# Kernel optimization log

Measured on AMD Instinct MI355X. Metric: run time of the kernel, lower is better.

The kernel has to match this reference:

```python
import jax, jax.numpy as jnp
import numpy as np

NUM_HEADS = 8
NUM_GROUPS = 32
EPS = 1e-5


def setup_inputs() -> dict:
    key = jax.random.key(0)
    k1, k2, k3 = jax.random.split(key, 3)
    B, C, H, W = 2, 512, 64, 64
    x = jax.random.normal(k1, (B, C, H, W), dtype=jnp.float32)
    gn_weight = jnp.ones((C,), dtype=jnp.float32)
    gn_bias = jnp.zeros((C,), dtype=jnp.float32)
    # small init so softmax logits are well-conditioned
    w_qkv = jax.random.normal(k2, (3 * C, C), dtype=jnp.float32) * 0.02
    w_proj = jax.random.normal(k3, (C, C), dtype=jnp.float32) * 0.02
    b_proj = jnp.zeros((C,), dtype=jnp.float32)
    return {"x": x, "gn_weight": gn_weight, "gn_bias": gn_bias,
            "w_qkv": w_qkv, "w_proj": w_proj, "b_proj": b_proj}


def group_norm(x, weight, bias):
    B, C, H, W = x.shape
    xg = x.reshape(B, NUM_GROUPS, C // NUM_GROUPS, H, W)
    mean = xg.mean(axis=(2, 3, 4), keepdims=True)
    var = xg.var(axis=(2, 3, 4), keepdims=True)
    xg = (xg - mean) * jax.lax.rsqrt(var + EPS)
    x = xg.reshape(B, C, H, W)
    return x * weight[None, :, None, None] + bias[None, :, None, None]


def reference(x, gn_weight, gn_bias, w_qkv, w_proj, b_proj):
    B, C, H, W = x.shape
    nh = NUM_HEADS
    hd = C // nh
    N = H * W

    h = group_norm(x, gn_weight, gn_bias)
    # 1x1 conv == per-pixel matmul: [B,3C,H,W]
    qkv = jnp.einsum('bchw,oc->bohw', h, w_qkv)
    # (B,3,nh,hd,N) -> (3,B,nh,N,hd)
    qkv = qkv.reshape(B, 3, nh, hd, N).transpose(1, 0, 2, 4, 3)
    q, k, v = qkv[0], qkv[1], qkv[2]

    scale = hd ** -0.5
    attn = jax.nn.softmax(jnp.einsum('bhnd,bhmd->bhnm', q, k) * scale, axis=-1)
    out = jnp.einsum('bhnm,bhmd->bhnd', attn, v)  # [B,nh,N,hd]
    out = out.transpose(0, 1, 3, 2).reshape(B, C, H, W)
    out = jnp.einsum('bchw,oc->bohw', out, w_proj) + b_proj[None, :, None, None]
    return x + out
```

## Files before the change

kernel.cpp:

```cpp
#include <hip/hip_runtime.h>
#include <math.h>

#define BB 2
#define CC 512
#define NN 4096
#define NH 8
#define HD 64
#define NG 32
#define CPG 16

typedef __attribute__((ext_vector_type(8))) short short8;
typedef __attribute__((ext_vector_type(4))) float f32x4;
typedef __attribute__((ext_vector_type(16))) float f32x16;

typedef __attribute__((address_space(1))) void glb_t;
typedef __attribute__((address_space(3))) void lds_t;

__device__ __forceinline__ void async16(const void* g, void* l) {
  __builtin_amdgcn_global_load_lds((const glb_t*)g, (lds_t*)l, 16, 0, 0);
}

__device__ __forceinline__ unsigned short f2bf(float f) {
  unsigned int u = __float_as_uint(f);
  u += 0x7fffu + ((u >> 16) & 1u);
  return (unsigned short)(u >> 16);
}

__device__ __forceinline__ unsigned int cvt_pk_bf16(float a, float b) {
  unsigned int r;
  asm("v_cvt_pk_bf16_f32 %0, %1, %2" : "=v"(r) : "v"(a), "v"(b));
  return r;
}

__global__ __launch_bounds__(256) void k_pre(const float* __restrict__ x,
                                             const float* __restrict__ wqkv,
                                             const float* __restrict__ wproj,
                                             float* __restrict__ stats,
                                             unsigned short* __restrict__ wb) {
  int bid = blockIdx.x;
  if (bid >= 64) {
    int i = ((bid - 64) * 256 + threadIdx.x) * 4;
    const float* src = (i < 786432) ? (wqkv + i) : (wproj + (i - 786432));
    float4 v = *(const float4*)src;
    ushort4 o;
    o.x = f2bf(v.x); o.y = f2bf(v.y); o.z = f2bf(v.z); o.w = f2bf(v.w);
    *(ushort4*)(wb + i) = o;
    return;
  }
  int b = bid >> 5, g = bid & 31;
  const float4* p = (const float4*)(x + (size_t)(b * CC + g * CPG) * NN);
  double s = 0.0, sq = 0.0;
  for (int i = threadIdx.x; i < (CPG * NN) / 4; i += 256) {
    float4 v = p[i];
    s  += (double)v.x + (double)v.y + (double)v.z + (double)v.w;
    sq += (double)v.x * v.x + (double)v.y * v.y + (double)v.z * v.z + (double)v.w * v.w;
  }
  __shared__ double red[512];
  red[threadIdx.x] = s; red[256 + threadIdx.x] = sq;
  __syncthreads();
  for (int off = 128; off > 0; off >>= 1) {
    if (threadIdx.x < off) {
      red[threadIdx.x] += red[threadIdx.x + off];
      red[256 + threadIdx.x] += red[256 + threadIdx.x + off];
    }
    __syncthreads();
  }
  if (threadIdx.x == 0) {
    double mean = red[0] / (double)(CPG * NN);
    double var  = red[256] / (double)(CPG * NN) - mean * mean;
    stats[(b * NG + g) * 2]     = (float)mean;
    stats[(b * NG + g) * 2 + 1] = (float)(1.0 / sqrt(var + 1e-5));
  }
}

__global__ __launch_bounds__(256) void k_gnapply(const float* __restrict__ x,
                                                 const float* __restrict__ gw,
                                                 const float* __restrict__ gb,
                                                 const float* __restrict__ stats,
                                                 unsigned short* __restrict__ hT) {
  int bid = blockIdx.x;
  int b = bid >> 9;
  int c0 = ((bid >> 6) & 7) * 64;
  int n0 = (bid & 63) * 64;
  __shared__ float tile[64 * 68];
  int t = threadIdx.x;
#pragma unroll
  for (int i = 0; i < 4; ++i) {
    int idx = i * 256 + t;
    int c = idx >> 4, n4 = (idx & 15) * 4;
    int cg = c0 + c, g = cg >> 4;
    float mu = stats[(b * NG + g) * 2], rs = stats[(b * NG + g) * 2 + 1];
    float w = gw[cg], bb = gb[cg];
    float4 v = *(const float4*)(x + (size_t)(b * CC + cg) * NN + n0 + n4);
    float* dst = tile + c * 68 + n4;
    dst[0] = (v.x - mu) * rs * w + bb;
    dst[1] = (v.y - mu) * rs * w + bb;
    dst[2] = (v.z - mu) * rs * w + bb;
    dst[3] = (v.w - mu) * rs * w + bb;
  }
  __syncthreads();
#pragma unroll
  for (int i = 0; i < 2; ++i) {
    int idx = i * 256 + t;
    int n = idx >> 3, c8 = (idx & 7) * 8;
    short8 o;
#pragma unroll
    for (int j = 0; j < 8; ++j) o[j] = (short)f2bf(tile[(c8 + j) * 68 + n]);
    *(short8*)(hT + (size_t)(b * NN + n0 + n) * CC + c0 + c8) = o;
  }
}

__device__ __forceinline__ void gemm_mainloop(const unsigned short* __restrict__ A,
                                              const unsigned short* __restrict__ Bm,
                                              char* smem, int m0, int n0,
                                              f32x4 acc[4][4]) {
  const int t = threadIdx.x, wave = t >> 6, lane = t & 63;
  const int l15 = lane & 15, lhi = lane >> 4;
  const int wr = wave >> 1, wc = wave & 1;
  const f32x4 fz = {0.f, 0.f, 0.f, 0.f};
#pragma unroll
  for (int mi = 0; mi < 4; ++mi)
#pragma unroll
    for (int ni = 0; ni < 4; ++ni) acc[mi][ni] = fz;

  for (int kt = 0; kt < 8; ++kt) {
    __syncthreads();
#pragma unroll
    for (int issue = 0; issue < 4; ++issue) {
      int slot = issue * 256 + t;
      int row = slot >> 3, g = slot & 7;
      async16(A + (size_t)(m0 + row) * 512 + kt * 64 + g * 8,
              smem + issue * 4096 + wave * 1024);
      async16(Bm + (size_t)(n0 + row) * 512 + kt * 64 + g * 8,
              smem + 16384 + issue * 4096 + wave * 1024);
    }
    __syncthreads();
#pragma unroll
    for (int kk = 0; kk < 2; ++kk) {
      short8 a[4], bf[4];
#pragma unroll
      for (int mi = 0; mi < 4; ++mi)
        a[mi] = *(const short8*)(smem + (wr * 64 + mi * 16 + l15) * 128 + kk * 64 + lhi * 16);
#pragma unroll
      for (int ni = 0; ni < 4; ++ni)
        bf[ni] = *(const short8*)(smem + 16384 + (wc * 64 + ni * 16 + l15) * 128 + kk * 64 + lhi * 16);
#pragma unroll
      for (int mi = 0; mi < 4; ++mi)
#pragma unroll
        for (int ni = 0; ni < 4; ++ni)
          acc[mi][ni] = __builtin_amdgcn_mfma_f32_16x16x32_bf16(a[mi], bf[ni], acc[mi][ni], 0, 0, 0);
    }
  }
}

__global__ __launch_bounds__(256) void k_qkvgemm(const unsigned short* __restrict__ hT,
                                                 const unsigned short* __restrict__ Wq,
                                                 unsigned short* __restrict__ Qp,
                                                 unsigned short* __restrict__ Kp,
                                                 unsigned short* __restrict__ Vp) {
  __shared__ char smem[32768];
  f32x4 acc[4][4];
  int m0 = blockIdx.x * 128, n0 = blockIdx.y * 128;
  gemm_mainloop(hT, Wq, smem, m0, n0, acc);
  const int t = threadIdx.x, wave = t >> 6, lane = t & 63;
  const int l15 = lane & 15, lhi = lane >> 4;
  const int wr = wave >> 1, wc = wave & 1;
  const int type = n0 >> 9;
  const int h0 = (n0 >> 6) & 7;
  __syncthreads();
  unsigned short* lim = (unsigned short*)smem;
  const float qs = 0.18033688011112042f;
#pragma unroll
  for (int mi = 0; mi < 4; ++mi)
#pragma unroll
    for (int ni = 0; ni < 4; ++ni)
#pragma unroll
      for (int r = 0; r < 4; ++r) {
        int pr = wr * 64 + mi * 16 + lhi * 4 + r;
        int oc = wc * 64 + ni * 16 + l15;
        int hh = oc >> 6, c = oc & 63;
        int tt2 = pr >> 6, pn = pr & 63;
        int idx;
        if (type < 2)
          idx = ((hh * 2 + tt2) * 8 + ((pn >> 5) << 2) + (c >> 4)) * 512
              + ((c >> 3) & 1) * 256 + (pn & 31) * 8 + (c & 7);
        else
          idx = ((hh * 2 + tt2) * 8 + ((pn >> 5) << 2) + (((pn >> 4) & 1) << 1) + (c >> 5)) * 512
              + ((pn >> 3) & 1) * 256 + (c & 31) * 8 + (pn & 7);
        float v = acc[mi][ni][r];
        if (type == 0) v *= qs;
        lim[idx] = f2bf(v);
      }
  __syncthreads();
  unsigned short* gbp = type == 0 ? Qp : (type == 1 ? Kp : Vp);
  int b = m0 >> 12, tile0 = (m0 & 4095) >> 6;
#pragma unroll
  for (int i = 0; i < 8; ++i) {
    int cidx = i * 256 + t;
    int pg = cidx >> 6;
    int bh = b * 8 + h0 + (pg >> 4);
    size_t dst = (size_t)bh * 262144 + (size_t)(tile0 + ((pg >> 3) & 1)) * 4096
               + (size_t)(pg & 7) * 512 + (size_t)(cidx & 63) * 8;
    *(short8*)(gbp + dst) = *(const short8*)(lim + cidx * 8);
  }
}

__global__ __launch_bounds__(256) void k_attn(const unsigned short* __restrict__ Qp,
                                              const unsigned short* __restrict__ Kp,
                                              const unsigned short* __restrict__ Vp,
                                              unsigned short* __restrict__ att) {
  __shared__ char smem[32768];
  const int t = threadIdx.x, wave = t >> 6, lane = t & 63;
  const int l31 = lane & 31, lh = lane >> 5;
  const int wq = wave >> 1, wk = wave & 1;
  int bid0 = blockIdx.x;
  int bid = (bid0 & 7) * 128 + (bid0 >> 3);
  int bh = bid >> 6, qt = bid & 63;
  int b = bh >> 3, h = bh & 7;

  const char* kCur = (const char*)Kp + (size_t)bh * 524288;
  const char* vCur = (const char*)Vp + (size_t)bh * 524288;
  const char* qSrc = (const char*)Qp + (size_t)bh * 524288 + (size_t)qt * 8192;

#pragma unroll
  for (int i = 0; i < 2; ++i) {
    int p = i * 4 + wave;
    async16(qSrc + p * 1024 + lane * 16, smem + 16384 + p * 1024);
    async16(kCur + p * 1024 + lane * 16, smem + p * 1024);
    async16(vCur + p * 1024 + lane * 16, smem + 8192 + p * 1024);
  }
  kCur += 8192; vCur += 8192;

  const int rbK = wk * 4096 + lane * 16;
  const int rbV = 8192 + wk * 4096 + lane * 16;
  const int rbQ = 16384 + wq * 4096 + lane * 16;

  __syncthreads();
  short8 qa[4];
#pragma unroll
  for (int kk = 0; kk < 4; ++kk)
    qa[kk] = *(const short8*)(smem + rbQ + kk * 1024);
  __syncthreads();

  f32x16 o0 = (f32x16)0.f, o1 = (f32x16)0.f;
  float lsum = 0.f;

#define ATTN_BODY(CURB, NXTB)                                                          \
  {                                                                                    \
    _Pragma("unroll")                                                                  \
    for (int i = 0; i < 2; ++i) {                                                      \
      int p = i * 4 + wave;                                                            \
      async16(kCur + p * 1024 + lane * 16, smem + (NXTB) + p * 1024);                  \
      async16(vCur + p * 1024 + lane * 16, smem + (NXTB) + 8192 + p * 1024);           \
    }                                                                                  \
    kCur += 8192; vCur += 8192;                                                        \
    f32x16 sT = (f32x16)0.f;                                                           \
    __builtin_amdgcn_s_setprio(1);                                                     \
    _Pragma("unroll")                                                                  \
    for (int kk = 0; kk < 4; ++kk) {                                                   \
      short8 ka = *(const short8*)(smem + (CURB) + rbK + kk * 1024);                   \
      sT = __builtin_amdgcn_mfma_f32_32x32x16_bf16(ka, qa[kk], sT, 0, 0, 0);           \
    }                                                                                  \
    __builtin_amdgcn_s_setprio(0);                                                     \
    float ls0 = 0.f, ls1 = 0.f;                                                        \
    _Pragma("unroll")                                                                  \
    for (int r = 0; r < 16; r += 2) {                                                  \
      sT[r]     = __builtin_amdgcn_exp2f(sT[r]);                                       \
      sT[r + 1] = __builtin_amdgcn_exp2f(sT[r + 1]);                                   \
      ls0 += sT[r]; ls1 += sT[r + 1];                                                  \
    }                                                                                  \
    lsum += ls0 + ls1;                                                                 \
    __builtin_amdgcn_s_setprio(1);                                                     \
    _Pragma("unroll")                                                                  \
    for (int kc = 0; kc < 2; ++kc) {                                                   \
      int rb = kc * 8;                                                                 \
      unsigned int x0 = cvt_pk_bf16(sT[rb],     sT[rb + 1]);                           \
      unsigned int x1 = cvt_pk_bf16(sT[rb + 2], sT[rb + 3]);                           \
      unsigned int x2 = cvt_pk_bf16(sT[rb + 4], sT[rb + 5]);                           \
      unsigned int x3 = cvt_pk_bf16(sT[rb + 6], sT[rb + 7]);                           \
      asm("v_permlane32_swap_b32 %0, %1" : "+v"(x0), "+v"(x2));                        \
      asm("v_permlane32_swap_b32 %0, %1" : "+v"(x1), "+v"(x3));                        \
      union { unsigned int d[4]; short8 s; } pb;                                       \
      pb.d[0] = x0; pb.d[1] = x1; pb.d[2] = x2; pb.d[3] = x3;                          \
      short8 va0 = *(const short8*)(smem + (CURB) + rbV + kc * 2048);                  \
      o0 = __builtin_amdgcn_mfma_f32_32x32x16_bf16(va0, pb.s, o0, 0, 0, 0);            \
      short8 va1 = *(const short8*)(smem + (CURB) + rbV + kc * 2048 + 1024);           \
      o1 = __builtin_amdgcn_mfma_f32_32x32x16_bf16(va1, pb.s, o1, 0, 0, 0);            \
    }                                                                                  \
    __builtin_amdgcn_s_setprio(0);                                                     \
    __syncthreads();                                                                   \
  }

  for (int it2 = 0; it2 < 32; ++it2) {
    ATTN_BODY(0, 16384)
    ATTN_BODY(16384, 0)
  }
#undef ATTN_BODY

  lsum += __shfl_xor(lsum, 32, 64);
  if (wk) {
    char* os = smem + wq * 8192;
#pragma unroll
    for (int dt = 0; dt < 2; ++dt)
#pragma unroll
      for (int rp = 0; rp < 4; ++rp) {
        f32x4 v;
        v[0] = (dt ? o1 : o0)[4 * rp];     v[1] = (dt ? o1 : o0)[4 * rp + 1];
        v[2] = (dt ? o1 : o0)[4 * rp + 2]; v[3] = (dt ? o1 : o0)[4 * rp + 3];
        *(f32x4*)(os + (dt * 4 + rp) * 1024 + lane * 16) = v;
      }
    *(float*)(smem + 16384 + wq * 256 + lane * 4) = lsum;
  }
  __syncthreads();
  if (!wk) {
    float lt = lsum + *(const float*)(smem + 16384 + wq * 256 + lane * 4);
    float rl = 1.f / lt;
    const char* os = smem + wq * 8192;
#pragma unroll
    for (int dt = 0; dt < 2; ++dt)
#pragma unroll
      for (int rp = 0; rp < 4; ++rp) {
        f32x4 v = *(const f32x4*)(os + (dt * 4 + rp) * 1024 + lane * 16);
        if (dt) {
          o1[4 * rp] += v[0]; o1[4 * rp + 1] += v[1];
          o1[4 * rp + 2] += v[2]; o1[4 * rp + 3] += v[3];
        } else {
          o0[4 * rp] += v[0]; o0[4 * rp + 1] += v[1];
          o0[4 * rp + 2] += v[2]; o0[4 * rp + 3] += v[3];
        }
      }
    unsigned short* abase = att + (size_t)(b * NN + qt * 64 + wq * 32 + l31) * CC + h * 64 + 4 * lh;
#pragma unroll
    for (int dt = 0; dt < 2; ++dt)
#pragma unroll
      for (int rp = 0; rp < 8; ++rp) {
        float e0 = (dt ? o1 : o0)[2 * rp], e1 = (dt ? o1 : o0)[2 * rp + 1];
        unsigned int w = cvt_pk_bf16(e0 * rl, e1 * rl);
        *(unsigned int*)(abase + 32 * dt + 8 * (rp >> 1) + 2 * (rp & 1)) = w;
      }
  }
}

__global__ __launch_bounds__(256) void k_projgemm(const unsigned short* __restrict__ att,
                                                  const unsigned short* __restrict__ Wp,
                                                  const float* __restrict__ x,
                                                  const float* __restrict__ bproj,
                                                  float* __restrict__ out) {
  __shared__ char smem[33280];
  f32x4 acc[4][4];
  int m0 = blockIdx.x * 128, n0 = blockIdx.y * 128;
  gemm_mainloop(att, Wp, smem, m0, n0, acc);
  const int t = threadIdx.x, wave = t >> 6, lane = t & 63;
  const int l15 = lane & 15, lhi = lane >> 4;
  const int wr = wave >> 1, wc = wave & 1;
  __syncthreads();
  float* stg = (float*)(smem + wave * 8320);
  int b = m0 >> 12;
  int nbase = (m0 & 4095) + wr * 64;
#pragma unroll
  for (int half = 0; half < 2; ++half) {
#pragma unroll
    for (int nl = 0; nl < 2; ++nl) {
      int ni = half * 2 + nl;
#pragma unroll
      for (int mi = 0; mi < 4; ++mi)
#pragma unroll
        for (int r = 0; r < 4; ++r) {
          int cl = nl * 16 + l15;
          int row = mi * 16 + lhi * 4 + r;
          stg[cl * 65 + row] = acc[mi][ni][r];
        }
    }
#pragma unroll 4
    for (int i = 0; i < 32; ++i) {
      int oc = n0 + wc * 64 + half * 32 + i;
      float v = stg[i * 65 + lane];
      size_t idx = (size_t)(b * CC + oc) * NN + nbase + lane;
      out[idx] = x[idx] + v + bproj[oc];
    }
    __syncthreads();
  }
}

extern "C" void kernel_launch(void* const* d_in, const int* in_sizes, int n_in,
                              void* d_out, int out_size, void* d_ws, size_t ws_size,
                              hipStream_t stream) {
  const float* x     = (const float*)d_in[0];
  const float* gw    = (const float*)d_in[1];
  const float* gb    = (const float*)d_in[2];
  const float* wqkv  = (const float*)d_in[3];
  const float* wproj = (const float*)d_in[4];
  const float* bproj = (const float*)d_in[5];
  float* out = (float*)d_out;
  char* ws = (char*)d_ws;

  unsigned short* Qp     = (unsigned short*)(ws + 0);
  unsigned short* Kp     = (unsigned short*)(ws + 8388608);
  unsigned short* Vp     = (unsigned short*)(ws + 16777216);
  unsigned short* hTb    = (unsigned short*)(ws + 25165824);
  unsigned short* attb   = (unsigned short*)(ws + 25165824);
  unsigned short* wqkvb  = (unsigned short*)(ws + 33554432);
  unsigned short* wprojb = (unsigned short*)(ws + 35127296);
  float*          stats  = (float*)(ws + 35651584);

  k_pre<<<1088, 256, 0, stream>>>(x, wqkv, wproj, stats, wqkvb);
  k_gnapply<<<1024, 256, 0, stream>>>(x, gw, gb, stats, hTb);
  k_qkvgemm<<<dim3(64, 12), 256, 0, stream>>>(hTb, wqkvb, Qp, Kp, Vp);
  k_attn<<<1024, 256, 0, stream>>>(Qp, Kp, Vp, attb);
  k_projgemm<<<dim3(64, 4), 256, 0, stream>>>(attb, wprojb, x, bproj, out);
}
```

Measured before the change: 235.8 us.

## Restructure attention: per-wave private K/V buffers, 64 queries per wave, no block barriers

Each wave now streams its own half of K/V into a private double-buffered LDS region and processes two 32-row query tiles (A and B) against each loaded K/V chunk. That halves the K/V traffic per query and drops the per-iteration __syncthreads, relying on explicit vmcnt/lgkmcnt waits instead. The grid is halved to 512 blocks, each covering 128 queries, and LDS grows to about 68KB with launch bounds targeting 2 blocks per CU. The cost is higher register pressure from four accumulators, fewer resident waves, and the risk that the hand-placed waitcnt ordering is fragile.

```diff
diff --git a/kernel.cpp b/kernel.cpp
--- a/kernel.cpp
+++ b/kernel.cpp
@@ -205,139 +205,189 @@
   }
 }
 
-__global__ __launch_bounds__(256) void k_attn(const unsigned short* __restrict__ Qp,
-                                              const unsigned short* __restrict__ Kp,
-                                              const unsigned short* __restrict__ Vp,
-                                              unsigned short* __restrict__ att) {
-  __shared__ char smem[32768];
+__global__ __launch_bounds__(256, 2) void k_attn(const unsigned short* __restrict__ Qp,
+                                                 const unsigned short* __restrict__ Kp,
+                                                 const unsigned short* __restrict__ Vp,
+                                                 unsigned short* __restrict__ att) {
+  __shared__ char smem[69632];
   const int t = threadIdx.x, wave = t >> 6, lane = t & 63;
   const int l31 = lane & 31, lh = lane >> 5;
-  const int wq = wave >> 1, wk = wave & 1;
+  const int qw = wave >> 1, wk = wave & 1;
   int bid0 = blockIdx.x;
-  int bid = (bid0 & 7) * 128 + (bid0 >> 3);
-  int bh = bid >> 6, qt = bid & 63;
+  int xcd = bid0 & 7, rr = bid0 >> 3;
+  int bh = xcd * 2 + (rr >> 5), qp = rr & 31;
+  int qt = qp * 2 + qw;
   int b = bh >> 3, h = bh & 7;
 
-  const char* kCur = (const char*)Kp + (size_t)bh * 524288;
-  const char* vCur = (const char*)Vp + (size_t)bh * 524288;
-  const char* qSrc = (const char*)Qp + (size_t)bh * 524288 + (size_t)qt * 8192;
-
-#pragma unroll
-  for (int i = 0; i < 2; ++i) {
-    int p = i * 4 + wave;
-    async16(qSrc + p * 1024 + lane * 16, smem + 16384 + p * 1024);
-    async16(kCur + p * 1024 + lane * 16, smem + p * 1024);
-    async16(vCur + p * 1024 + lane * 16, smem + 8192 + p * 1024);
-  }
-  kCur += 8192; vCur += 8192;
-
-  const int rbK = wk * 4096 + lane * 16;
-  const int rbV = 8192 + wk * 4096 + lane * 16;
-  const int rbQ = 16384 + wq * 4096 + lane * 16;
-
-  __syncthreads();
-  short8 qa[4];
-#pragma unroll
-  for (int kk = 0; kk < 4; ++kk)
-    qa[kk] = *(const short8*)(smem + rbQ + kk * 1024);
-  __syncthreads();
-
-  f32x16 o0 = (f32x16)0.f, o1 = (f32x16)0.f;
-  float lsum = 0.f;
-
-#define ATTN_BODY(CURB, NXTB)                                                          \
+  char* myLds = smem + wave * 16384;
+  const char* kPtr = (const char*)Kp + (size_t)bh * 524288 + wk * 4096 + lane * 16;
+  const char* vPtr = (const char*)Vp + (size_t)bh * 524288 + wk * 4096 + lane * 16;
+  const char* qPtr = (const char*)Qp + (size_t)bh * 524288 + (size_t)qt * 8192 + lane * 16;
+
+#pragma unroll
+  for (int j = 0; j < 4; ++j) {
+    async16(qPtr + j * 1024, myLds + 8192 + j * 1024);
+    async16(qPtr + 4096 + j * 1024, myLds + 12288 + j * 1024);
+  }
+#pragma unroll
+  for (int j = 0; j < 4; ++j) {
+    async16(kPtr + j * 1024, myLds + j * 1024);
+    async16(vPtr + j * 1024, myLds + 4096 + j * 1024);
+  }
+  kPtr += 8192; vPtr += 8192;
+  asm volatile("s_waitcnt vmcnt(8)" ::: "memory");
+  __builtin_amdgcn_sched_barrier(0);
+  short8 qaA[4], qaB[4];
+#pragma unroll
+  for (int kk = 0; kk < 4; ++kk) {
+    qaA[kk] = *(const short8*)(myLds + 8192 + kk * 1024 + lane * 16);
+    qaB[kk] = *(const short8*)(myLds + 12288 + kk * 1024 + lane * 16);
+  }
+  asm volatile("s_waitcnt lgkmcnt(0)" ::: "memory");
+  __builtin_amdgcn_sched_barrier(0);
+
+  const f32x16 fz = (f32x16)0.f;
+  f32x16 oA0 = fz, oA1 = fz, oB0 = fz, oB1 = fz;
+  float lsA = 0.f, lsB = 0.f;
+
+#define BODY(CURB, NXTB)                                                               \
   {                                                                                    \
+    asm volatile("s_waitcnt lgkmcnt(0)" ::: "memory");      \
+    __builtin_amdgcn_sched_barrier(0);                                                 \
     _Pragma("unroll")                                                                  \
-    for (int i = 0; i < 2; ++i) {                                                      \
-      int p = i * 4 + wave;                                                            \
-      async16(kCur + p * 1024 + lane * 16, smem + (NXTB) + p * 1024);                  \
-      async16(vCur + p * 1024 + lane * 16, smem + (NXTB) + 8192 + p * 1024);           \
-    }                                                                                  \
-    kCur += 8192; vCur += 8192;                                                        \
-    f32x16 sT = (f32x16)0.f;                                                           \
+    for (int j = 0; j < 4; ++j) {                                                      \
+      async16(kPtr + j * 1024, myLds + (NXTB) + j * 1024);                             \
+      async16(vPtr + j * 1024, myLds + (NXTB) + 4096 + j * 1024);                      \
+    }                                                                                  \
+    kPtr += 8192; vPtr += 8192;                                                        \
+    asm volatile("s_waitcnt vmcnt(8)" ::: "memory");       \
+    __builtin_amdgcn_sched_barrier(0);                                                 \
+    f32x16 sA, sB;                                                                     \
     __builtin_amdgcn_s_setprio(1);                                                     \
-    _Pragma("unroll")                                                                  \
-    for (int kk = 0; kk < 4; ++kk) {                                                   \
-      short8 ka = *(const short8*)(smem + (CURB) + rbK + kk * 1024);                   \
-      sT = __builtin_amdgcn_mfma_f32_32x32x16_bf16(ka, qa[kk], sT, 0, 0, 0);           \
+    {                                                                                  \
+      short8 ka = *(const short8*)(myLds + (CURB) + lane * 16);                        \
+      sA = __builtin_amdgcn_mfma_f32_32x32x16_bf16(ka, qaA[0], fz, 0, 0, 0);           \
+      sB = __builtin_amdgcn_mfma_f32_32x32x16_bf16(ka, qaB[0], fz, 0, 0, 0);           \
+      ka = *(const short8*)(myLds + (CURB) + 1024 + lane * 16);                        \
+      sA = __builtin_amdgcn_mfma_f32_32x32x16_bf16(ka, qaA[1], sA, 0, 0, 0);           \
+      sB = __builtin_amdgcn_mfma_f32_32x32x16_bf16(ka, qaB[1], sB, 0, 0, 0);           \
+      ka = *(const short8*)(myLds + (CURB) + 2048 + lane * 16);                        \
+      sA = __builtin_amdgcn_mfma_f32_32x32x16_bf16(ka, qaA[2], sA, 0, 0, 0);           \
+      sB = __builtin_amdgcn_mfma_f32_32x32x16_bf16(ka, qaB[2], sB, 0, 0, 0);           \
+      ka = *(const short8*)(myLds + (CURB) + 3072 + lane * 16);                        \
+      sA = __builtin_amdgcn_mfma_f32_32x32x16_bf16(ka, qaA[3], sA, 0, 0, 0);           \
+      sB = __builtin_amdgcn_mfma_f32_32x32x16_bf16(ka, qaB[3], sB, 0, 0, 0);           \
     }                                                                                  \
     __builtin_amdgcn_s_setprio(0);                                                     \
-    float ls0 = 0.f, ls1 = 0.f;                                                        \
+    short8 va0 = *(const short8*)(myLds + (CURB) + 4096 + lane * 16);                  \
+    short8 va1 = *(const short8*)(myLds + (CURB) + 5120 + lane * 16);                  \
+    short8 va2 = *(const short8*)(myLds + (CURB) + 6144 + lane * 16);                  \
+    short8 va3 = *(const short8*)(myLds + (CURB) + 7168 + lane * 16);                  \
+    float g0 = 0.f, g1 = 0.f;                                                          \
     _Pragma("unroll")                                                                  \
     for (int r = 0; r < 16; r += 2) {                                                  \
-      sT[r]     = __builtin_amdgcn_exp2f(sT[r]);                                       \
-      sT[r + 1] = __builtin_amdgcn_exp2f(sT[r + 1]);                                   \
-      ls0 += sT[r]; ls1 += sT[r + 1];                                                  \
-    }                                                                                  \
-    lsum += ls0 + ls1;                                                                 \
+      sA[r]     = __builtin_amdgcn_exp2f(sA[r]);                                       \
+      sA[r + 1] = __builtin_amdgcn_exp2f(sA[r + 1]);                                   \
+      g0 += sA[r]; g1 += sA[r + 1];                                                    \
+    }                                                                                  \
+    lsA += g0 + g1;                                                                    \
     __builtin_amdgcn_s_setprio(1);                                                     \
     _Pragma("unroll")                                                                  \
     for (int kc = 0; kc < 2; ++kc) {                                                   \
       int rb = kc * 8;                                                                 \
-      unsigned int x0 = cvt_pk_bf16(sT[rb],     sT[rb + 1]);                           \
-      unsigned int x1 = cvt_pk_bf16(sT[rb + 2], sT[rb + 3]);                           \
-      unsigned int x2 = cvt_pk_bf16(sT[rb + 4], sT[rb + 5]);                           \
-      unsigned int x3 = cvt_pk_bf16(sT[rb + 6], sT[rb + 7]);                           \
+      unsigned int x0 = cvt_pk_bf16(sA[rb],     sA[rb + 1]);                           \
+      unsigned int x1 = cvt_pk_bf16(sA[rb + 2], sA[rb + 3]);                           \
+      unsigned int x2 = cvt_pk_bf16(sA[rb + 4], sA[rb + 5]);                           \
+      unsigned int x3 = cvt_pk_bf16(sA[rb + 6], sA[rb + 7]);                           \
       asm("v_permlane32_swap_b32 %0, %1" : "+v"(x0), "+v"(x2));                        \
       asm("v_permlane32_swap_b32 %0, %1" : "+v"(x1), "+v"(x3));                        \
       union { unsigned int d[4]; short8 s; } pb;                                       \
       pb.d[0] = x0; pb.d[1] = x1; pb.d[2] = x2; pb.d[3] = x3;                          \
-      short8 va0 = *(const short8*)(smem + (CURB) + rbV + kc * 2048);                  \
-      o0 = __builtin_amdgcn_mfma_f32_32x32x16_bf16(va0, pb.s, o0, 0, 0, 0);            \
-      short8 va1 = *(const short8*)(smem + (CURB) + rbV + kc * 2048 + 1024);           \
-      o1 = __builtin_amdgcn_mfma_f32_32x32x16_bf16(va1, pb.s, o1, 0, 0, 0);            \
+      oA0 = __builtin_amdgcn_mfma_f32_32x32x16_bf16(kc ? va2 : va0, pb.s, oA0, 0, 0, 0); \
+      oA1 = __builtin_amdgcn_mfma_f32_32x32x16_bf16(kc ? va3 : va1, pb.s, oA1, 0, 0, 0); \
     }                                                                                  \
     __builtin_amdgcn_s_setprio(0);                                                     \
-    __syncthreads();                                                                   \
+    g0 = 0.f; g1 = 0.f;                                                                \
+    _Pragma("unroll")                                                                  \
+    for (int r = 0; r < 16; r += 2) {                                                  \
+      sB[r]     = __builtin_amdgcn_exp2f(sB[r]);                                       \
+      sB[r + 1] = __builtin_amdgcn_exp2f(sB[r + 1]);                                   \
+      g0 += sB[r]; g1 += sB[r + 1];                                                    \
+    }                                                                                  \
+    lsB += g0 + g1;                                                                    \
+    __builtin_amdgcn_s_setprio(1);                                                     \
+    _Pragma("unroll")                                                                  \
+    for (int kc = 0; kc < 2; ++kc) {                                                   \
+      int rb = kc * 8;                                                                 \
+      unsigned int x0 = cvt_pk_bf16(sB[rb],     sB[rb + 1]);                           \
+      unsigned int x1 = cvt_pk_bf16(sB[rb + 2], sB[rb + 3]);                           \
+      unsigned int x2 = cvt_pk_bf16(sB[rb + 4], sB[rb + 5]);                           \
+      unsigned int x3 = cvt_pk_bf16(sB[rb + 6], sB[rb + 7]);                           \
+      asm("v_permlane32_swap_b32 %0, %1" : "+v"(x0), "+v"(x2));                        \
+      asm("v_permlane32_swap_b32 %0, %1" : "+v"(x1), "+v"(x3));                        \
+      union { unsigned int d[4]; short8 s; } pb;                                       \
+      pb.d[0] = x0; pb.d[1] = x1; pb.d[2] = x2; pb.d[3] = x3;                          \
+      oB0 = __builtin_amdgcn_mfma_f32_32x32x16_bf16(kc ? va2 : va0, pb.s, oB0, 0, 0, 0); \
+      oB1 = __builtin_amdgcn_mfma_f32_32x32x16_bf16(kc ? va3 : va1, pb.s, oB1, 0, 0, 0); \
+    }                                                                                  \
+    __builtin_amdgcn_s_setprio(0);                                                     \
   }
 
   for (int it2 = 0; it2 < 32; ++it2) {
-    ATTN_BODY(0, 16384)
-    ATTN_BODY(16384, 0)
-  }
-#undef ATTN_BODY
-
-  lsum += __shfl_xor(lsum, 32, 64);
+    BODY(0, 8192)
+    BODY(8192, 0)
+  }
+#undef BODY
+
+  lsA += __shfl_xor(lsA, 32, 64);
+  lsB += __shfl_xor(lsB, 32, 64);
+  __syncthreads();
   if (wk) {
-    char* os = smem + wq * 8192;
-#pragma unroll
-    for (int dt = 0; dt < 2; ++dt)
-#pragma unroll
-      for (int rp = 0; rp < 4; ++rp) {
-        f32x4 v;
-        v[0] = (dt ? o1 : o0)[4 * rp];     v[1] = (dt ? o1 : o0)[4 * rp + 1];
-        v[2] = (dt ? o1 : o0)[4 * rp + 2]; v[3] = (dt ? o1 : o0)[4 * rp + 3];
-        *(f32x4*)(os + (dt * 4 + rp) * 1024 + lane * 16) = v;
+#pragma unroll
+    for (int c = 0; c < 4; ++c) {
+      f32x4 w;
+      w[0] = oA0[4 * c]; w[1] = oA0[4 * c + 1]; w[2] = oA0[4 * c + 2]; w[3] = oA0[4 * c + 3];
+      *(f32x4*)(myLds + c * 1024 + lane * 16) = w;
+      w[0] = oA1[4 * c]; w[1] = oA1[4 * c + 1]; w[2] = oA1[4 * c + 2]; w[3] = oA1[4 * c + 3];
+      *(f32x4*)(myLds + 4096 + c * 1024 + lane * 16) = w;
+      w[0] = oB0[4 * c]; w[1] = oB0[4 * c + 1]; w[2] = oB0[4 * c + 2]; w[3] = oB0[4 * c + 3];
+      *(f32x4*)(myLds + 8192 + c * 1024 + lane * 16) = w;
+      w[0] = oB1[4 * c]; w[1] = oB1[4 * c + 1]; w[2] = oB1[4 * c + 2]; w[3] = oB1[4 * c + 3];
+      *(f32x4*)(myLds + 12288 + c * 1024 + lane * 16) = w;
+    }
+    float2 lp; lp.x = lsA; lp.y = lsB;
+    *(float2*)(smem + 65536 + wave * 512 + lane * 8) = lp;
+  }
+  __syncthreads();
+  if (!wk) {
+    const char* ps = myLds + 16384;
+#pragma unroll
+    for (int c = 0; c < 4; ++c) {
+      f32x4 v0 = *(const f32x4*)(ps + c * 1024 + lane * 16);
+      f32x4 v1 = *(const f32x4*)(ps + 4096 + c * 1024 + lane * 16);
+      f32x4 v2 = *(const f32x4*)(ps + 8192 + c * 1024 + lane * 16);
+      f32x4 v3 = *(const f32x4*)(ps + 12288 + c * 1024 + lane * 16);
+#pragma unroll
+      for (int i = 0; i < 4; ++i) {
+        oA0[4 * c + i] += v0[i];
+        oA1[4 * c + i] += v1[i];
+        oB0[4 * c + i] += v2[i];
+        oB1[4 * c + i] += v3[i];
       }
-    *(float*)(smem + 16384 + wq * 256 + lane * 4) = lsum;
-  }
-  __syncthreads();
-  if (!wk) {
-    float lt = lsum + *(const float*)(smem + 16384 + wq * 256 + lane * 4);
-    float rl = 1.f / lt;
-    const char* os = smem + wq * 8192;
-#pragma unroll
-    for (int dt = 0; dt < 2; ++dt)
-#pragma unroll
-      for (int rp = 0; rp < 4; ++rp) {
-        f32x4 v = *(const f32x4*)(os + (dt * 4 + rp) * 1024 + lane * 16);
-        if (dt) {
-          o1[4 * rp] += v[0]; o1[4 * rp + 1] += v[1];
-          o1[4 * rp + 2] += v[2]; o1[4 * rp + 3] += v[3];
-        } else {
-          o0[4 * rp] += v[0]; o0[4 * rp + 1] += v[1];
-          o0[4 * rp + 2] += v[2]; o0[4 * rp + 3] += v[3];
-        }
-      }
-    unsigned short* abase = att + (size_t)(b * NN + qt * 64 + wq * 32 + l31) * CC + h * 64 + 4 * lh;
-#pragma unroll
-    for (int dt = 0; dt < 2; ++dt)
-#pragma unroll
-      for (int rp = 0; rp < 8; ++rp) {
-        float e0 = (dt ? o1 : o0)[2 * rp], e1 = (dt ? o1 : o0)[2 * rp + 1];
-        unsigned int w = cvt_pk_bf16(e0 * rl, e1 * rl);
-        *(unsigned int*)(abase + 32 * dt + 8 * (rp >> 1) + 2 * (rp & 1)) = w;
-      }
+    }
+    float2 lp = *(const float2*)(smem + 65536 + (wave + 1) * 512 + lane * 8);
+    float rlA = 1.f / (lsA + lp.x);
+    float rlB = 1.f / (lsB + lp.y);
+    unsigned short* aA = att + (size_t)(b * NN + qt * 64 + l31) * CC + h * 64 + 4 * lh;
+    unsigned short* aB = att + (size_t)(b * NN + qt * 64 + 32 + l31) * CC + h * 64 + 4 * lh;
+#pragma unroll
+    for (int rp = 0; rp < 8; ++rp) {
+      int off = 8 * (rp >> 1) + 2 * (rp & 1);
+      *(unsigned int*)(aA + off)      = cvt_pk_bf16(oA0[2 * rp] * rlA, oA0[2 * rp + 1] * rlA);
+      *(unsigned int*)(aA + 32 + off) = cvt_pk_bf16(oA1[2 * rp] * rlA, oA1[2 * rp + 1] * rlA);
+      *(unsigned int*)(aB + off)      = cvt_pk_bf16(oB0[2 * rp] * rlB, oB0[2 * rp + 1] * rlB);
+      *(unsigned int*)(aB + 32 + off) = cvt_pk_bf16(oB1[2 * rp] * rlB, oB1[2 * rp + 1] * rlB);
+    }
   }
 }
 
@@ -406,6 +456,6 @@
   k_pre<<<1088, 256, 0, stream>>>(x, wqkv, wproj, stats, wqkvb);
   k_gnapply<<<1024, 256, 0, stream>>>(x, gw, gb, stats, hTb);
   k_qkvgemm<<<dim3(64, 12), 256, 0, stream>>>(hTb, wqkvb, Qp, Kp, Vp);
-  k_attn<<<1024, 256, 0, stream>>>(Qp, Kp, Vp, attb);
+  k_attn<<<512, 256, 0, stream>>>(Qp, Kp, Vp, attb);
   k_projgemm<<<dim3(64, 4), 256, 0, stream>>>(attb, wprojb, x, bproj, out);
 }
```

Result: faster. 224.0 us (-5.0%).
